# Performance work log

Hardware: AMD Instinct MI355X
Metric: run time of the kernel (lower is better)

The kernel has to match this reference:

```python
import jax, jax.numpy as jnp
import numpy as np

B, H, T = 32, 48, 24
S, A, R, F, L = 256, 64, 8, 1024, 2
EPS = 1e-5


def setup_inputs() -> dict:
    key = jax.random.key(0)
    ks = jax.random.split(key, 12)
    def w(k, shape):
        fan_in = shape[-1]
        return jax.random.normal(k, shape, jnp.float32) / jnp.sqrt(jnp.float32(fan_in))
    return {
        'history_s': jax.random.normal(ks[0], (B, H, S), jnp.float32),
        'history_a': jax.random.normal(ks[1], (B, H, A), jnp.float32),
        'present_s': jax.random.normal(ks[2], (B, S), jnp.float32),
        'future_s': jax.random.normal(ks[3], (B, T, S), jnp.float32),
        'future_a': jax.random.normal(ks[4], (B, T, A), jnp.float32),
        'W_state': w(ks[5], (F, S)), 'b_state': jnp.zeros((F,), jnp.float32),
        'g_sn': jnp.ones((F,), jnp.float32), 'b_sn': jnp.zeros((F,), jnp.float32),
        'W_action': w(ks[6], (F, A)), 'b_action': jnp.zeros((F,), jnp.float32),
        'g_an': jnp.ones((F,), jnp.float32), 'b_an': jnp.zeros((F,), jnp.float32),
        'gru_Wi': w(ks[7], (L, 3 * F, F)), 'gru_Wh': w(ks[8], (L, 3 * F, F)),
        'gru_bi': jnp.zeros((L, 3 * F), jnp.float32), 'gru_bh': jnp.zeros((L, 3 * F), jnp.float32),
        'W_reward': w(ks[9], (R, F)), 'b_reward': jnp.zeros((R,), jnp.float32),
        'W_sout': w(ks[10], (S, F)), 'b_sout': jnp.zeros((S,), jnp.float32),
    }


def _ln(x, g, b):
    m = jnp.mean(x, axis=-1, keepdims=True)
    v = jnp.mean(jnp.square(x - m), axis=-1, keepdims=True)
    return (x - m) / jnp.sqrt(v + EPS) * g + b


def _gelu(x):
    return jax.nn.gelu(x, approximate=False)  # torch F.gelu default = exact erf


def _gru_step(Wi, Wh, bi, bh, hs, x):
    # hs: [L,B,F] hidden per layer; x: [B,F]. PyTorch GRU cell semantics.
    new_hs = []
    inp = x
    for l in range(Wi.shape[0]):
        gi = inp @ Wi[l].T + bi[l]      # [B,3F]
        gh = hs[l] @ Wh[l].T + bh[l]    # [B,3F]
        ir, iz, inn = jnp.split(gi, 3, axis=-1)
        hr, hz, hn = jnp.split(gh, 3, axis=-1)
        r = jax.nn.sigmoid(ir + hr)
        z = jax.nn.sigmoid(iz + hz)
        n = jnp.tanh(inn + r * hn)
        h_new = (1.0 - z) * n + z * hs[l]
        new_hs.append(h_new)
        inp = h_new  # dropout between layers is identity (drop_rate=0)
    return jnp.stack(new_hs), inp


def reference(history_s, history_a, present_s, future_s, future_a,
              W_state, b_state, g_sn, b_sn, W_action, b_action, g_an, b_an,
              gru_Wi, gru_Wh, gru_bi, gru_bh, W_reward, b_reward, W_sout, b_sout):
    # Original forward() reruns the GRU from scratch over a growing window each
    # future step; since h0=0 this is mathematically identical to carrying the
    # hidden state incrementally (module's own _forward variant), which we do.
    Bv = history_s.shape[0]
    Fv = W_state.shape[0]
    Lv = gru_Wi.shape[0]

    hs = _ln(history_s @ W_state.T + b_state, g_sn, b_sn)   # [B,H,F]
    ha = _ln(history_a @ W_action.T + b_action, g_an, b_an)  # [B,H,F]
    ps = _ln(present_s @ W_state.T + b_state, g_sn, b_sn)    # [B,F]
    fa = _ln(future_a @ W_action.T + b_action, g_an, b_an)   # [B,T,F]

    hist_sa = hs + ha  # [B,H,F]

    def head(y):
        r = jnp.tanh(y @ W_reward.T + b_reward)
        s = y @ W_sout.T + b_sout  # state_activation is identity
        return r, s

    # step 0: full window = history + (present + future_a[0])
    seq0 = _gelu(jnp.concatenate([hist_sa, (ps + fa[:, 0])[:, None, :]], axis=1))
    h0 = jnp.zeros((Lv, Bv, Fv), seq0.dtype)

    def scan_seq(h, x):
        h, y = _gru_step(gru_Wi, gru_Wh, gru_bi, gru_bh, h, x)
        return h, y

    hT, ys = jax.lax.scan(scan_seq, h0, jnp.swapaxes(seq0, 0, 1))  # ys: [H+1,B,F]
    r0, s0 = head(ys[-1])
    pres = _ln(s0 @ W_state.T + b_state, g_sn, b_sn)

    def scan_fut(carry, fa_t):
        h, p = carry
        x = _gelu(p + fa_t)  # [B,F]
        h, y = _gru_step(gru_Wi, gru_Wh, gru_bi, gru_bh, h, x)
        r, s = head(y)
        p_new = _ln(s @ W_state.T + b_state, g_sn, b_sn)
        return (h, p_new), (r, s)

    _, (rs, ss) = jax.lax.scan(scan_fut, (hT, pres), jnp.swapaxes(fa[:, 1:], 0, 1))
    future_r = jnp.concatenate([r0[:, None], jnp.swapaxes(rs, 0, 1)], axis=1)  # [B,T,R]
    future_s_out = jnp.concatenate([s0[:, None], jnp.swapaxes(ss, 0, 1)], axis=1)  # [B,T,S]
    return future_r, future_s_out
```

## Files before the change

### kernel.cpp

```cpp
#include <hip/hip_runtime.h>
#include <cmath>

constexpr int kB = 32, kH = 48, kT = 24, kS = 256, kA = 64, kR = 8, kF = 1024;
constexpr int kSEQ = kH + 1;
constexpr float kEPS = 1e-5f;

constexpr int G  = 128;
constexpr int BT = 512;

typedef __attribute__((ext_vector_type(8))) short short8;
typedef __attribute__((ext_vector_type(4))) float f32x4;

union U4S8 { uint4 u; short8 s; };

__device__ __forceinline__ unsigned bfbits(float x) {
  unsigned u = __float_as_uint(x);
  return (u + 0x7fffu + ((u >> 16) & 1u)) >> 16;
}
__device__ __forceinline__ float bf_lo(unsigned u) { return __uint_as_float(u << 16); }
__device__ __forceinline__ float bf_hi(unsigned u) { return __uint_as_float(u & 0xffff0000u); }
__device__ __forceinline__ float bf2f(unsigned short h) {
  return __uint_as_float(((unsigned)h) << 16);
}
__device__ __forceinline__ float gelu_f(float x) {
  return 0.5f * x * (1.0f + erff(x * 0.7071067811865476f));
}
__device__ __forceinline__ float sigmoid_f(float x) {
  return 1.0f / (1.0f + expf(-x));
}

__device__ __forceinline__ void coh_st(unsigned* p, unsigned v) {
  __hip_atomic_store(p, v, __ATOMIC_RELAXED, __HIP_MEMORY_SCOPE_AGENT);
}

__device__ __forceinline__ void wwait(const unsigned* line, unsigned tgt) {
  for (;;) {
    unsigned v;
    asm volatile("global_load_dword %0, %1, off sc0 sc1\n\t"
                 "s_waitcnt vmcnt(0)"
                 : "=v"(v) : "v"(line) : "memory");
    if (v >= tgt) break;
    __builtin_amdgcn_s_sleep(1);
  }
}
__device__ __forceinline__ void wait4(const unsigned* fl,
                                      unsigned t0, unsigned t1,
                                      unsigned t2, unsigned t3) {
  if (threadIdx.x == 0) {
    for (;;) {
      unsigned a, b, c, d;
      asm volatile(
        "global_load_dword %0, %4, off sc0 sc1\n\t"
        "global_load_dword %1, %5, off sc0 sc1\n\t"
        "global_load_dword %2, %6, off sc0 sc1\n\t"
        "global_load_dword %3, %7, off sc0 sc1\n\t"
        "s_waitcnt vmcnt(0)"
        : "=&v"(a), "=&v"(b), "=&v"(c), "=&v"(d)
        : "v"(fl), "v"(fl + 32), "v"(fl + 64), "v"(fl + 96)
        : "memory");
      if (a >= t0 && b >= t1 && c >= t2 && d >= t3) break;
      __builtin_amdgcn_s_sleep(1);
    }
  }
  __syncthreads();
}
__device__ __forceinline__ void sig_oct(unsigned* fl, int fb) {
  if (threadIdx.x == 0)
    __hip_atomic_fetch_add(fl + ((fb >> 3) & 7) * 32, 1u,
                           __ATOMIC_RELAXED, __HIP_MEMORY_SCOPE_AGENT);
}
__device__ __forceinline__ void sig16(unsigned* fl, int b) {
  if (threadIdx.x == 0)
    __hip_atomic_fetch_add(fl + ((b >> 4) & 1) * 32, 1u,
                           __ATOMIC_RELAXED, __HIP_MEMORY_SCOPE_AGENT);
}

__device__ __forceinline__ void layer_stage(
    const unsigned short* __restrict__ xsrc,
    const unsigned short* __restrict__ hsrc,
    unsigned short* __restrict__ hdst,
    const unsigned* xw8,
    const unsigned* hw8,
    const unsigned* xblk2,
    int hfirst,
    const short8 (&Bf)[2][3][4],
    float bR, float bZ, float bIN, float bHN,
    float& h_old, float* part, int fb)
{
  const int tid = threadIdx.x;
  const int wv = tid >> 6, l = tid & 63, q = l >> 4, c = l & 15;

  short8 Ax[2][4], Ah[2][4];
  const int base = c*1024 + wv*128 + q*8;

  if (hfirst) {
    if (hw8) wwait(hw8 + wv*32, 8u);
    #pragma unroll
    for (int mt = 0; mt < 2; mt++)
      #pragma unroll
      for (int j = 0; j < 4; j++)
        Ah[mt][j] = *(const short8*)(hsrc + base + mt*16*1024 + j*32);
    if (xblk2) wait4(xblk2, 16u, 16u, 0u, 0u);
    if (xw8) wwait(xw8 + wv*32, 8u);
    #pragma unroll
    for (int mt = 0; mt < 2; mt++)
      #pragma unroll
      for (int j = 0; j < 4; j++)
        Ax[mt][j] = *(const short8*)(xsrc + base + mt*16*1024 + j*32);
  } else {
    #pragma unroll
    for (int mt = 0; mt < 2; mt++)
      #pragma unroll
      for (int j = 0; j < 4; j++)
        Ax[mt][j] = *(const short8*)(xsrc + base + mt*16*1024 + j*32);
    if (hw8) wwait(hw8 + wv*32, 8u);
    #pragma unroll
    for (int mt = 0; mt < 2; mt++)
      #pragma unroll
      for (int j = 0; j < 4; j++)
        Ah[mt][j] = *(const short8*)(hsrc + base + mt*16*1024 + j*32);
  }

  f32x4 C[4][2];
  #pragma unroll
  for (int s = 0; s < 4; s++)
    #pragma unroll
    for (int mt = 0; mt < 2; mt++)
      C[s][mt] = (f32x4){0.f, 0.f, 0.f, 0.f};

  #pragma unroll
  for (int mt = 0; mt < 2; mt++)
    #pragma unroll
    for (int j = 0; j < 4; j++) {
      C[0][mt] = __builtin_amdgcn_mfma_f32_16x16x32_bf16(Ax[mt][j], Bf[0][0][j], C[0][mt], 0, 0, 0);
      C[0][mt] = __builtin_amdgcn_mfma_f32_16x16x32_bf16(Ah[mt][j], Bf[1][0][j], C[0][mt], 0, 0, 0);
      C[1][mt] = __builtin_amdgcn_mfma_f32_16x16x32_bf16(Ax[mt][j], Bf[0][1][j], C[1][mt], 0, 0, 0);
      C[1][mt] = __builtin_amdgcn_mfma_f32_16x16x32_bf16(Ah[mt][j], Bf[1][1][j], C[1][mt], 0, 0, 0);
      C[2][mt] = __builtin_amdgcn_mfma_f32_16x16x32_bf16(Ax[mt][j], Bf[0][2][j], C[2][mt], 0, 0, 0);
      C[3][mt] = __builtin_amdgcn_mfma_f32_16x16x32_bf16(Ah[mt][j], Bf[1][2][j], C[3][mt], 0, 0, 0);
    }

  const int perm = (wv + l + (l >> 3)) & 7;
  #pragma unroll
  for (int s = 0; s < 4; s++)
    #pragma unroll
    for (int mt = 0; mt < 2; mt++)
      #pragma unroll
      for (int r = 0; r < 4; r++)
        part[((s*2 + mt)*4 + r)*512 + l*8 + perm] = C[s][mt][r];
  __syncthreads();

  const int mt_c = wv & 1, rg = wv >> 1;
  const int b_own = mt_c*16 + q*4 + rg;
  float S[4];
  #pragma unroll
  for (int s = 0; s < 4; s++) {
    const float* pp = part + ((s*2 + mt_c)*4 + rg)*512 + l*8;
    f32x4 a = *(const f32x4*)pp;
    f32x4 b = *(const f32x4*)(pp + 4);
    S[s] = ((a[0]+a[1]) + (a[2]+a[3])) + ((b[0]+b[1]) + (b[2]+b[3]));
  }
  float rr = sigmoid_f(S[0] + bR);
  float zz = sigmoid_f(S[1] + bZ);
  float nn = tanhf(S[2] + bIN + rr * (S[3] + bHN));
  float hn = (1.f - zz)*nn + zz*h_old;
  h_old = hn;
  float nb = __shfl_xor(hn, 1);
  if (!(c & 1)) {
    unsigned pk = bfbits(hn) | (bfbits(nb) << 16);
    coh_st((unsigned*)(hdst + b_own*1024 + fb*16 + c), pk);
  }
  __syncthreads();
}

__device__ __forceinline__ void f3_stage(
    const unsigned short* __restrict__ y_bf, int t,
    const unsigned short* __restrict__ WsT2_bf, const float* __restrict__ b_sout,
    const unsigned short* __restrict__ Wr_bf, const float* __restrict__ b_reward,
    const unsigned short* __restrict__ WstT_bf, const float* __restrict__ b_state,
    const float* __restrict__ g_sn, const float* __restrict__ b_sn,
    const unsigned short* __restrict__ fa_bf,
    float* __restrict__ out_r, float* __restrict__ out_s,
    unsigned short* __restrict__ xbuf_bf, float* part, int b)
{
  const int tid = threadIdx.x;
  float* yb    = part;
  float* spart = part + 1024;
  float* s_sh  = part + 1536;
  float* rpart = part + 1792;
  float* red1  = part + 2048;
  float* red2  = part + 2560;

  {
    unsigned uu = *((const unsigned*)y_bf + b*512 + tid);
    yb[tid*2]     = bf_lo(uu);
    yb[tid*2 + 1] = bf_hi(uu);
  }
  __syncthreads();
  {
    const int j = tid & 255, ksh = tid >> 8;
    const unsigned* wp = (const unsigned*)WsT2_bf + (size_t)ksh*256*256 + j;
    const float* yp = yb + ksh*512;
    float acc = 0.f;
    #pragma unroll 8
    for (int kp = 0; kp < 256; kp++) {
      unsigned w = wp[kp*256];
      acc += bf_lo(w)*yp[2*kp] + bf_hi(w)*yp[2*kp + 1];
    }
    spart[tid] = acc;
  }
  __syncthreads();
  if (tid < 256) {
    float s = spart[tid] + spart[tid + 256] + b_sout[tid];
    out_s[((size_t)b*kT + t)*kS + tid] = s;
    s_sh[tid] = s;
  } else if (tid < 320) {
    const int idx = tid - 256, j = idx >> 3, ks = idx & 7;
    const unsigned short* wr = Wr_bf + j*1024 + ks*128;
    const float* yp = yb + ks*128;
    float acc = 0.f;
    #pragma unroll 4
    for (int k = 0; k < 128; k += 2) {
      unsigned w = *(const unsigned*)(wr + k);
      acc += bf_lo(w)*yp[k] + bf_hi(w)*yp[k+1];
    }
    rpart[idx] = acc;
  }
  __syncthreads();
  if (tid < 8) {
    float a = b_reward[tid];
    #pragma unroll
    for (int ks = 0; ks < 8; ks++) a += rpart[tid*8 + ks];
    out_r[((size_t)b*kT + t)*kR + tid] = tanhf(a);
  }
  if (t == kT - 1) return;
  __syncthreads();
  const int f0 = tid*2;
  float a0 = b_state[f0], a1 = b_state[f0 + 1];
  {
    const unsigned* wp = (const unsigned*)WstT_bf + (f0 >> 1);
    #pragma unroll 8
    for (int k = 0; k < 256; k++) {
      unsigned w = wp[k*512];
      a0 += bf_lo(w)*s_sh[k];
      a1 += bf_hi(w)*s_sh[k];
    }
  }
  float s1 = a0 + a1, s2 = a0*a0 + a1*a1;
  red1[tid] = s1; red2[tid] = s2;
  __syncthreads();
  for (int off = 256; off > 0; off >>= 1) {
    if (tid < off) { red1[tid] += red1[tid + off]; red2[tid] += red2[tid + off]; }
    __syncthreads();
  }
  const float mean = red1[0] * (1.0f/kF);
  const float var  = red2[0] * (1.0f/kF) - mean*mean;
  const float inv  = rsqrtf(var + kEPS);
  unsigned fu = *((const unsigned*)(fa_bf + ((size_t)(t+1)*kB + b)*kF) + tid);
  float x0 = (a0 - mean)*inv*g_sn[f0]   + b_sn[f0]   + bf_lo(fu);
  float x1 = (a1 - mean)*inv*g_sn[f0+1] + b_sn[f0+1] + bf_hi(fu);
  unsigned pk = bfbits(gelu_f(x0)) | (bfbits(gelu_f(x1)) << 16);
  coh_st((unsigned*)xbuf_bf + b*512 + tid, pk);
}

__device__ __forceinline__ void load_bfrags(
    const float* __restrict__ gru_Wi, const float* __restrict__ gru_Wh,
    int lay, int fb, int wv, int q, int c, short8 (&Bf)[2][3][4])
{
  const size_t WLL = (size_t)3 * kF * kF;
  const float* Wm[2] = { gru_Wi + lay*WLL, gru_Wh + lay*WLL };
  #pragma unroll
  for (int m = 0; m < 2; m++)
    #pragma unroll
    for (int g = 0; g < 3; g++)
      #pragma unroll
      for (int j = 0; j < 4; j++) {
        const float* p = Wm[m] + ((size_t)(g*kF + fb*16 + c))*kF + wv*128 + j*32 + q*8;
        float4 a = *(const float4*)p;
        float4 b = *(const float4*)(p + 4);
        U4S8 u;
        u.u.x = bfbits(a.x) | (bfbits(a.y) << 16);
        u.u.y = bfbits(a.z) | (bfbits(a.w) << 16);
        u.u.z = bfbits(b.x) | (bfbits(b.y) << 16);
        u.u.w = bfbits(b.z) | (bfbits(b.w) << 16);
        Bf[m][g][j] = u.s;
      }
}

__global__ __launch_bounds__(BT, 2) void gru_hist(
    const float* __restrict__ gru_Wi, const float* __restrict__ gru_Wh,
    const float* __restrict__ gru_bi, const float* __restrict__ gru_bh,
    const unsigned short* __restrict__ seq0_bf,
    unsigned short* h0pool, unsigned short* h1pool,
    unsigned* hflags)
{
  __shared__ float part[32 * 512];
  const int tid = threadIdx.x;
  const int blk = blockIdx.x;
  const int wv = tid >> 6, l = tid & 63, q = l >> 4, c = l & 15;
  const bool isL1 = (blk >= 64);
  const int fb = blk & 63;
  const int lay = isL1 ? 1 : 0;
  const size_t BF = (size_t)kB * kF;

  short8 Bf[2][3][4];
  load_bfrags(gru_Wi, gru_Wh, lay, fb, wv, q, c, Bf);
  const int f = fb*16 + c;
  const float* bi = gru_bi + lay*3*kF;
  const float* bh = gru_bh + lay*3*kF;
  const float bR  = bi[f] + bh[f];
  const float bZ  = bi[kF + f] + bh[kF + f];
  const float bIN = bi[2*kF + f];
  const float bHN = bh[2*kF + f];

  float h_old = 0.f;

  #define H0P(i) (h0pool + (size_t)(i)*BF)
  #define H1P(i) (h1pool + (size_t)(i)*BF)
  #define FH0(s) (hflags + (size_t)((s) - 1) * 256)
  #define FH1(s) (hflags + (size_t)(48 + (s)) * 256)

  for (int s = 0; s < 50; s++) {
    if (!isL1) {
      if (s < 49) {
        layer_stage(seq0_bf + (size_t)s*BF, H0P(s), H0P(s+1),
                    nullptr, (s >= 1) ? FH0(s) : nullptr, nullptr, 0,
                    Bf, bR, bZ, bIN, bHN, h_old, part, fb);
        sig_oct(FH0(s+1), fb);
      }
    } else {
      if (s >= 1) {
        layer_stage(H0P(s), H1P(s-1), H1P(s),
                    FH0(s), (s >= 2) ? FH1(s-1) : nullptr, nullptr, 1,
                    Bf, bR, bZ, bIN, bHN, h_old, part, fb);
        sig_oct(FH1(s), fb);
      }
    }
  }
  #undef H0P
  #undef H1P
  #undef FH0
  #undef FH1
}

__global__ __launch_bounds__(BT, 2) void gru_fut(
    const float* __restrict__ gru_Wi, const float* __restrict__ gru_Wh,
    const float* __restrict__ gru_bi, const float* __restrict__ gru_bh,
    const unsigned short* __restrict__ WsT2_bf, const float* __restrict__ b_sout,
    const unsigned short* __restrict__ Wr_bf, const float* __restrict__ b_reward,
    const unsigned short* __restrict__ WstT_bf, const float* __restrict__ b_state,
    const float* __restrict__ g_sn, const float* __restrict__ b_sn,
    const unsigned short* __restrict__ fa_bf,
    unsigned short* h0pool, unsigned short* h1pool, unsigned short* xbpool,
    unsigned* fflags,
    float* __restrict__ out_r, float* __restrict__ out_s)
{
  __shared__ float part[32 * 512];
  const int tid = threadIdx.x;
  const int blk = blockIdx.x;
  const int wv = tid >> 6, l = tid & 63, q = l >> 4, c = l & 15;
  const bool isL1 = (blk >= 64);
  const int fb = blk & 63;
  const int lay = isL1 ? 1 : 0;
  const size_t BF = (size_t)kB * kF;

  short8 Bf[2][3][4];
  load_bfrags(gru_Wi, gru_Wh, lay, fb, wv, q, c, Bf);
  const int f = fb*16 + c;
  const float* bi = gru_bi + lay*3*kF;
  const float* bh = gru_bh + lay*3*kF;
  const float bR  = bi[f] + bh[f];
  const float bZ  = bi[kF + f] + bh[kF + f];
  const float bIN = bi[2*kF + f];
  const float bHN = bh[2*kF + f];

  #define H0P(i) (h0pool + (size_t)(i)*BF)
  #define H1P(i) (h1pool + (size_t)(i)*BF)
  #define XBP(i) (xbpool + (size_t)(i)*BF)
  #define FH0F(t) (fflags + (size_t)(t) * 256)
  #define FH1F(t) (fflags + (size_t)(23 + (t)) * 256)
  #define FXF(t)  (fflags + (size_t)46 * 256 + (size_t)(t) * 64)

  const int b_own = (wv & 1)*16 + q*4 + (wv >> 1);
  float h_old;
  {
    const unsigned short* hs = isL1 ? H1P(49) : H0P(49);
    h_old = bf2f(hs[b_own*1024 + f]);
  }

  for (int t = 0; t < kT; t++) {
    if (blk < kB) {
      if (t >= 1) {
        wait4(FH1F(t-1), 8u, 8u, 8u, 8u);
        wait4(FH1F(t-1) + 128, 8u, 8u, 8u, 8u);
      }
      f3_stage(H1P(49+t), t, WsT2_bf, b_sout, Wr_bf, b_reward,
               WstT_bf, b_state, g_sn, b_sn, fa_bf,
               out_r, out_s, XBP(t), part, blk);
      if (t < kT - 1) { __syncthreads(); sig16(FXF(t), blk); }
    }
    if (t == kT - 1) break;
    if (!isL1) {
      layer_stage(XBP(t), H0P(49+t), H0P(50+t),
                  nullptr, (t >= 1) ? FH0F(t-1) : nullptr, FXF(t), 1,
                  Bf, bR, bZ, bIN, bHN, h_old, part, fb);
      sig_oct(FH0F(t), fb);
    } else {
      layer_stage(H0P(50+t), H1P(49+t), H1P(50+t),
                  FH0F(t), (t >= 1) ? FH1F(t-1) : nullptr, nullptr, 1,
                  Bf, bR, bZ, bIN, bHN, h_old, part, fb);
      sig_oct(FH1F(t), fb);
    }
  }
  #undef H0P
  #undef H1P
  #undef XBP
  #undef FH0F
  #undef FH1F
  #undef FXF
}

__global__ __launch_bounds__(512) void convert_weights(
    const float* __restrict__ ws,  unsigned short* __restrict__ wsT2,
    const float* __restrict__ wst, unsigned short* __restrict__ wstT,
    const float* __restrict__ wr,  unsigned short* __restrict__ o3)
{
  const int stride = gridDim.x * blockDim.x;
  const int i0 = blockIdx.x * blockDim.x + threadIdx.x;
  for (int i = i0; i < kS*kF; i += stride) {
    const int j = i >> 10, k = i & 1023;
    wsT2[(k >> 1)*512 + j*2 + (k & 1)] = (unsigned short)bfbits(ws[i]);
  }
  for (int i = i0; i < kF*kS; i += stride) {
    const int ff = i >> 8, k = i & 255;
    wstT[k*1024 + ff] = (unsigned short)bfbits(wst[i]);
  }
  for (int i = i0; i < kR*kF; i += stride) o3[i] = (unsigned short)bfbits(wr[i]);
}

__global__ __launch_bounds__(256) void encode_fa_kernel(
    const float* __restrict__ future_a,
    const float* __restrict__ W_action, const float* __restrict__ b_action,
    const float* __restrict__ g_an, const float* __restrict__ b_an,
    unsigned short* __restrict__ fa_bf)
{
  __shared__ __align__(16) float arow[kA];
  __shared__ float red1[256], red2[256];
  const int bid = blockIdx.x;
  const int b = bid & (kB - 1);
  const int t = bid >> 5;
  const int tid = threadIdx.x;
  if (tid < kA) arow[tid] = future_a[((size_t)b*kT + t)*kA + tid];
  __syncthreads();
  float v[4]; float s1 = 0.f, s2 = 0.f;
  #pragma unroll
  for (int j = 0; j < 4; j++) {
    const int ff = tid + j*256;
    const float* wr = W_action + (size_t)ff*kA;
    float acc = b_action[ff];
    for (int k = 0; k < kA; k += 4) {
      float4 w  = *(const float4*)(wr + k);
      float4 xv = *(const float4*)(arow + k);
      acc += xv.x*w.x + xv.y*w.y + xv.z*w.z + xv.w*w.w;
    }
    v[j] = acc; s1 += acc; s2 += acc*acc;
  }
  red1[tid] = s1; red2[tid] = s2;
  __syncthreads();
  for (int off = 128; off > 0; off >>= 1) {
    if (tid < off) { red1[tid] += red1[tid+off]; red2[tid] += red2[tid+off]; }
    __syncthreads();
  }
  const float m = red1[0] * (1.0f/kF);
  const float va = red2[0] * (1.0f/kF) - m*m;
  const float inv = rsqrtf(va + kEPS);
  #pragma unroll
  for (int j = 0; j < 4; j++) {
    const int ff = tid + j*256;
    fa_bf[((size_t)t*kB + b)*kF + ff] =
        (unsigned short)bfbits((v[j] - m)*inv*g_an[ff] + b_an[ff]);
  }
}

__global__ __launch_bounds__(256) void encode_seq0_kernel(
    const float* __restrict__ history_s, const float* __restrict__ history_a,
    const float* __restrict__ present_s,
    const float* __restrict__ W_state, const float* __restrict__ b_state,
    const float* __restrict__ g_sn, const float* __restrict__ b_sn,
    const float* __restrict__ W_action, const float* __restrict__ b_action,
    const float* __restrict__ g_an, const float* __restrict__ b_an,
    const unsigned short* __restrict__ fa_bf, unsigned short* __restrict__ seq0_bf)
{
  __shared__ __align__(16) float srow[kS];
  __shared__ __align__(16) float arow[kA];
  __shared__ float red1[256], red2[256];
  const int bid = blockIdx.x;
  const int b = bid & (kB - 1);
  const int t = bid >> 5;
  const int tid = threadIdx.x;
  const bool hist = (t < kH);
  const float* sp = hist ? (history_s + ((size_t)b*kH + t)*kS)
                         : (present_s + (size_t)b*kS);
  srow[tid] = sp[tid];
  if (hist && tid < kA) arow[tid] = history_a[((size_t)b*kH + t)*kA + tid];
  __syncthreads();

  float u[4]; float s1 = 0.f, s2 = 0.f;
  #pragma unroll
  for (int j = 0; j < 4; j++) {
    const int ff = tid + j*256;
    const float* wr = W_state + (size_t)ff*kS;
    float acc = b_state[ff];
    for (int k = 0; k < kS; k += 4) {
      float4 w  = *(const float4*)(wr + k);
      float4 xv = *(const float4*)(srow + k);
      acc += xv.x*w.x + xv.y*w.y + xv.z*w.z + xv.w*w.w;
    }
    u[j] = acc; s1 += acc; s2 += acc*acc;
  }
  red1[tid] = s1; red2[tid] = s2;
  __syncthreads();
  for (int off = 128; off > 0; off >>= 1) {
    if (tid < off) { red1[tid] += red1[tid+off]; red2[tid] += red2[tid+off]; }
    __syncthreads();
  }
  const float mu = red1[0] * (1.0f/kF);
  const float vu = red2[0] * (1.0f/kF) - mu*mu;
  const float iu = rsqrtf(vu + kEPS);
  __syncthreads();

  if (hist) {
    float v[4]; s1 = 0.f; s2 = 0.f;
    #pragma unroll
    for (int j = 0; j < 4; j++) {
      const int ff = tid + j*256;
      const float* wr = W_action + (size_t)ff*kA;
      float acc = b_action[ff];
      for (int k = 0; k < kA; k += 4) {
        float4 w  = *(const float4*)(wr + k);
        float4 xv = *(const float4*)(arow + k);
        acc += xv.x*w.x + xv.y*w.y + xv.z*w.z + xv.w*w.w;
      }
      v[j] = acc; s1 += acc; s2 += acc*acc;
    }
    red1[tid] = s1; red2[tid] = s2;
    __syncthreads();
    for (int off = 128; off > 0; off >>= 1) {
      if (tid < off) { red1[tid] += red1[tid+off]; red2[tid] += red2[tid+off]; }
      __syncthreads();
    }
    const float mv = red1[0] * (1.0f/kF);
    const float vv = red2[0] * (1.0f/kF) - mv*mv;
    const float iv = rsqrtf(vv + kEPS);
    #pragma unroll
    for (int j = 0; j < 4; j++) {
      const int ff = tid + j*256;
      const float un = (u[j] - mu)*iu*g_sn[ff] + b_sn[ff];
      const float vn = (v[j] - mv)*iv*g_an[ff] + b_an[ff];
      seq0_bf[((size_t)t*kB + b)*kF + ff] = (unsigned short)bfbits(gelu_f(un + vn));
    }
  } else {
    #pragma unroll
    for (int j = 0; j < 4; j++) {
      const int ff = tid + j*256;
      const float un = (u[j] - mu)*iu*g_sn[ff] + b_sn[ff];
      seq0_bf[((size_t)t*kB + b)*kF + ff] =
          (unsigned short)bfbits(gelu_f(un + bf2f(fa_bf[(size_t)b*kF + ff])));
    }
  }
}

extern "C" void kernel_launch(void* const* d_in, const int* in_sizes, int n_in,
                              void* d_out, int out_size, void* d_ws, size_t ws_size,
                              hipStream_t stream) {
  (void)in_sizes; (void)n_in; (void)out_size;
  const float* history_s = (const float*)d_in[0];
  const float* history_a = (const float*)d_in[1];
  const float* present_s = (const float*)d_in[2];
  const float* future_a  = (const float*)d_in[4];
  const float* W_state   = (const float*)d_in[5];
  const float* b_state   = (const float*)d_in[6];
  const float* g_sn      = (const float*)d_in[7];
  const float* b_sn      = (const float*)d_in[8];
  const float* W_action  = (const float*)d_in[9];
  const float* b_action  = (const float*)d_in[10];
  const float* g_an      = (const float*)d_in[11];
  const float* b_an      = (const float*)d_in[12];
  const float* gru_Wi    = (const float*)d_in[13];
  const float* gru_Wh    = (const float*)d_in[14];
  const float* gru_bi    = (const float*)d_in[15];
  const float* gru_bh    = (const float*)d_in[16];
  const float* W_reward  = (const float*)d_in[17];
  const float* b_reward  = (const float*)d_in[18];
  const float* W_sout    = (const float*)d_in[19];
  const float* b_sout    = (const float*)d_in[20];

  char* ws = (char*)d_ws;
  unsigned short* seq0_bf = (unsigned short*)(ws + 0);
  unsigned short* fa_bf   = (unsigned short*)(ws + 3211264);
  unsigned short* WsT2_bf = (unsigned short*)(ws + 4784128);
  unsigned short* WstT_bf = (unsigned short*)(ws + 5308416);
  unsigned short* Wr_bf   = (unsigned short*)(ws + 5832704);
  unsigned short* h0pool  = (unsigned short*)(ws + 5849088);
  unsigned short* h1pool  = (unsigned short*)(ws + 10633216);
  unsigned short* xbpool  = (unsigned short*)(ws + 15417344);
  unsigned*       hflags  = (unsigned*)(ws + 16924672);
  unsigned*       fflags  = (unsigned*)(ws + 17025024);
  const size_t need = 17078016;
  if (ws_size < need) return;

  hipMemsetAsync((void*)h0pool, 0, 65536, stream);
  hipMemsetAsync((void*)h1pool, 0, 65536, stream);
  hipMemsetAsync((void*)hflags, 0, 100352 + 52992, stream);

  float* out_r = (float*)d_out;
  float* out_s = out_r + (size_t)kB*kT*kR;

  hipLaunchKernelGGL(convert_weights, dim3(256), dim3(512), 0, stream,
                     W_sout, WsT2_bf, W_state, WstT_bf, W_reward, Wr_bf);
  hipLaunchKernelGGL(encode_fa_kernel, dim3(kT*kB), dim3(256), 0, stream,
                     future_a, W_action, b_action, g_an, b_an, fa_bf);
  hipLaunchKernelGGL(encode_seq0_kernel, dim3(kSEQ*kB), dim3(256), 0, stream,
                     history_s, history_a, present_s,
                     W_state, b_state, g_sn, b_sn,
                     W_action, b_action, g_an, b_an, fa_bf, seq0_bf);
  hipLaunchKernelGGL(gru_hist, dim3(G), dim3(BT), 0, stream,
                     gru_Wi, gru_Wh, gru_bi, gru_bh,
                     seq0_bf, h0pool, h1pool, hflags);
  hipLaunchKernelGGL(gru_fut, dim3(G), dim3(BT), 0, stream,
                     gru_Wi, gru_Wh, gru_bi, gru_bh,
                     WsT2_bf, b_sout, Wr_bf, b_reward, WstT_bf, b_state,
                     g_sn, b_sn, fa_bf,
                     h0pool, h1pool, xbpool, fflags,
                     out_r, out_s);
}
```

Measured before the change: 1.472 ms.

## Fuse head/state feedback into layer-0 blocks with MFMA and defer outputs

The future-step feedback path (y→s→state projection→LayerNorm→GELU) no longer runs in 32 dedicated blocks that signal the layer-0 blocks through a global buffer and flags. Each layer-0 block now recomputes it redundantly for all 32 batches using bf16 MFMA in LDS, which removes one cross-block synchronisation hop per timestep. Output heads for s and r are computed after the recurrence by otherwise idle blocks, overlapped with the remaining steps. The cost is much more redundant per-block compute and weight reads on the critical path, and occupancy drops to one block per CU.

```diff
diff --git a/kernel.cpp b/kernel.cpp
--- a/kernel.cpp
+++ b/kernel.cpp
@@ -27,6 +27,15 @@
 }
 __device__ __forceinline__ float sigmoid_f(float x) {
   return 1.0f / (1.0f + expf(-x));
+}
+__device__ __forceinline__ float dot8bb(const unsigned short* w, const unsigned short* y) {
+  uint4 a = *(const uint4*)w; uint4 b = *(const uint4*)y;
+  float r = 0.f;
+  r += bf_lo(a.x)*bf_lo(b.x); r += bf_hi(a.x)*bf_hi(b.x);
+  r += bf_lo(a.y)*bf_lo(b.y); r += bf_hi(a.y)*bf_hi(b.y);
+  r += bf_lo(a.z)*bf_lo(b.z); r += bf_hi(a.z)*bf_hi(b.z);
+  r += bf_lo(a.w)*bf_lo(b.w); r += bf_hi(a.w)*bf_hi(b.w);
+  return r;
 }
 
 __device__ __forceinline__ void coh_st(unsigned* p, unsigned v) {
@@ -69,19 +78,12 @@
     __hip_atomic_fetch_add(fl + ((fb >> 3) & 7) * 32, 1u,
                            __ATOMIC_RELAXED, __HIP_MEMORY_SCOPE_AGENT);
 }
-__device__ __forceinline__ void sig16(unsigned* fl, int b) {
-  if (threadIdx.x == 0)
-    __hip_atomic_fetch_add(fl + ((b >> 4) & 1) * 32, 1u,
-                           __ATOMIC_RELAXED, __HIP_MEMORY_SCOPE_AGENT);
-}
 
 __device__ __forceinline__ void layer_stage(
     const unsigned short* __restrict__ xsrc,
     const unsigned short* __restrict__ hsrc,
     unsigned short* __restrict__ hdst,
-    const unsigned* xw8,
-    const unsigned* hw8,
-    const unsigned* xblk2,
+    const unsigned* xw8, const unsigned* hw8,
     int hfirst,
     const short8 (&Bf)[2][3][4],
     float bR, float bZ, float bIN, float bHN,
@@ -100,7 +102,6 @@
       #pragma unroll
       for (int j = 0; j < 4; j++)
         Ah[mt][j] = *(const short8*)(hsrc + base + mt*16*1024 + j*32);
-    if (xblk2) wait4(xblk2, 16u, 16u, 0u, 0u);
     if (xw8) wwait(xw8 + wv*32, 8u);
     #pragma unroll
     for (int mt = 0; mt < 2; mt++)
@@ -171,96 +172,6 @@
     coh_st((unsigned*)(hdst + b_own*1024 + fb*16 + c), pk);
   }
   __syncthreads();
-}
-
-__device__ __forceinline__ void f3_stage(
-    const unsigned short* __restrict__ y_bf, int t,
-    const unsigned short* __restrict__ WsT2_bf, const float* __restrict__ b_sout,
-    const unsigned short* __restrict__ Wr_bf, const float* __restrict__ b_reward,
-    const unsigned short* __restrict__ WstT_bf, const float* __restrict__ b_state,
-    const float* __restrict__ g_sn, const float* __restrict__ b_sn,
-    const unsigned short* __restrict__ fa_bf,
-    float* __restrict__ out_r, float* __restrict__ out_s,
-    unsigned short* __restrict__ xbuf_bf, float* part, int b)
-{
-  const int tid = threadIdx.x;
-  float* yb    = part;
-  float* spart = part + 1024;
-  float* s_sh  = part + 1536;
-  float* rpart = part + 1792;
-  float* red1  = part + 2048;
-  float* red2  = part + 2560;
-
-  {
-    unsigned uu = *((const unsigned*)y_bf + b*512 + tid);
-    yb[tid*2]     = bf_lo(uu);
-    yb[tid*2 + 1] = bf_hi(uu);
-  }
-  __syncthreads();
-  {
-    const int j = tid & 255, ksh = tid >> 8;
-    const unsigned* wp = (const unsigned*)WsT2_bf + (size_t)ksh*256*256 + j;
-    const float* yp = yb + ksh*512;
-    float acc = 0.f;
-    #pragma unroll 8
-    for (int kp = 0; kp < 256; kp++) {
-      unsigned w = wp[kp*256];
-      acc += bf_lo(w)*yp[2*kp] + bf_hi(w)*yp[2*kp + 1];
-    }
-    spart[tid] = acc;
-  }
-  __syncthreads();
-  if (tid < 256) {
-    float s = spart[tid] + spart[tid + 256] + b_sout[tid];
-    out_s[((size_t)b*kT + t)*kS + tid] = s;
-    s_sh[tid] = s;
-  } else if (tid < 320) {
-    const int idx = tid - 256, j = idx >> 3, ks = idx & 7;
-    const unsigned short* wr = Wr_bf + j*1024 + ks*128;
-    const float* yp = yb + ks*128;
-    float acc = 0.f;
-    #pragma unroll 4
-    for (int k = 0; k < 128; k += 2) {
-      unsigned w = *(const unsigned*)(wr + k);
-      acc += bf_lo(w)*yp[k] + bf_hi(w)*yp[k+1];
-    }
-    rpart[idx] = acc;
-  }
-  __syncthreads();
-  if (tid < 8) {
-    float a = b_reward[tid];
-    #pragma unroll
-    for (int ks = 0; ks < 8; ks++) a += rpart[tid*8 + ks];
-    out_r[((size_t)b*kT + t)*kR + tid] = tanhf(a);
-  }
-  if (t == kT - 1) return;
-  __syncthreads();
-  const int f0 = tid*2;
-  float a0 = b_state[f0], a1 = b_state[f0 + 1];
-  {
-    const unsigned* wp = (const unsigned*)WstT_bf + (f0 >> 1);
-    #pragma unroll 8
-    for (int k = 0; k < 256; k++) {
-      unsigned w = wp[k*512];
-      a0 += bf_lo(w)*s_sh[k];
-      a1 += bf_hi(w)*s_sh[k];
-    }
-  }
-  float s1 = a0 + a1, s2 = a0*a0 + a1*a1;
-  red1[tid] = s1; red2[tid] = s2;
-  __syncthreads();
-  for (int off = 256; off > 0; off >>= 1) {
-    if (tid < off) { red1[tid] += red1[tid + off]; red2[tid] += red2[tid + off]; }
-    __syncthreads();
-  }
-  const float mean = red1[0] * (1.0f/kF);
-  const float var  = red2[0] * (1.0f/kF) - mean*mean;
-  const float inv  = rsqrtf(var + kEPS);
-  unsigned fu = *((const unsigned*)(fa_bf + ((size_t)(t+1)*kB + b)*kF) + tid);
-  float x0 = (a0 - mean)*inv*g_sn[f0]   + b_sn[f0]   + bf_lo(fu);
-  float x1 = (a1 - mean)*inv*g_sn[f0+1] + b_sn[f0+1] + bf_hi(fu);
-  unsigned pk = bfbits(gelu_f(x0)) | (bfbits(gelu_f(x1)) << 16);
-  coh_st((unsigned*)xbuf_bf + b*512 + tid, pk);
 }
 
 __device__ __forceinline__ void load_bfrags(
@@ -324,14 +235,14 @@
     if (!isL1) {
       if (s < 49) {
         layer_stage(seq0_bf + (size_t)s*BF, H0P(s), H0P(s+1),
-                    nullptr, (s >= 1) ? FH0(s) : nullptr, nullptr, 0,
+                    nullptr, (s >= 1) ? FH0(s) : nullptr, 0,
                     Bf, bR, bZ, bIN, bHN, h_old, part, fb);
         sig_oct(FH0(s+1), fb);
       }
     } else {
       if (s >= 1) {
         layer_stage(H0P(s), H1P(s-1), H1P(s),
-                    FH0(s), (s >= 2) ? FH1(s-1) : nullptr, nullptr, 1,
+                    FH0(s), (s >= 2) ? FH1(s-1) : nullptr, 1,
                     Bf, bR, bZ, bIN, bHN, h_old, part, fb);
         sig_oct(FH1(s), fb);
       }
@@ -343,19 +254,20 @@
   #undef FH1
 }
 
-__global__ __launch_bounds__(BT, 2) void gru_fut(
+__global__ __launch_bounds__(BT, 1) void gru_fut(
     const float* __restrict__ gru_Wi, const float* __restrict__ gru_Wh,
     const float* __restrict__ gru_bi, const float* __restrict__ gru_bh,
-    const unsigned short* __restrict__ WsT2_bf, const float* __restrict__ b_sout,
+    const unsigned short* __restrict__ Ws_bf, const float* __restrict__ b_sout,
     const unsigned short* __restrict__ Wr_bf, const float* __restrict__ b_reward,
-    const unsigned short* __restrict__ WstT_bf, const float* __restrict__ b_state,
+    const unsigned short* __restrict__ Wst_bf, const float* __restrict__ b_state,
     const float* __restrict__ g_sn, const float* __restrict__ b_sn,
     const unsigned short* __restrict__ fa_bf,
-    unsigned short* h0pool, unsigned short* h1pool, unsigned short* xbpool,
+    unsigned short* h0pool, unsigned short* h1pool,
     unsigned* fflags,
     float* __restrict__ out_r, float* __restrict__ out_s)
 {
   __shared__ float part[32 * 512];
+  unsigned short* lds_bf = (unsigned short*)part;
   const int tid = threadIdx.x;
   const int blk = blockIdx.x;
   const int wv = tid >> 6, l = tid & 63, q = l >> 4, c = l & 15;
@@ -376,10 +288,8 @@
 
   #define H0P(i) (h0pool + (size_t)(i)*BF)
   #define H1P(i) (h1pool + (size_t)(i)*BF)
-  #define XBP(i) (xbpool + (size_t)(i)*BF)
   #define FH0F(t) (fflags + (size_t)(t) * 256)
   #define FH1F(t) (fflags + (size_t)(23 + (t)) * 256)
-  #define FXF(t)  (fflags + (size_t)46 * 256 + (size_t)(t) * 64)
 
   const int b_own = (wv & 1)*16 + q*4 + (wv >> 1);
   float h_old;
@@ -388,53 +298,307 @@
     h_old = bf2f(hs[b_own*1024 + f]);
   }
 
-  for (int t = 0; t < kT; t++) {
-    if (blk < kB) {
-      if (t >= 1) {
-        wait4(FH1F(t-1), 8u, 8u, 8u, 8u);
-        wait4(FH1F(t-1) + 128, 8u, 8u, 8u, 8u);
-      }
-      f3_stage(H1P(49+t), t, WsT2_bf, b_sout, Wr_bf, b_reward,
-               WstT_bf, b_state, g_sn, b_sn, fa_bf,
-               out_r, out_s, XBP(t), part, blk);
-      if (t < kT - 1) { __syncthreads(); sig16(FXF(t), blk); }
-    }
-    if (t == kT - 1) break;
+  for (int t = 0; t < kT - 1; t++) {
     if (!isL1) {
-      layer_stage(XBP(t), H0P(49+t), H0P(50+t),
-                  nullptr, (t >= 1) ? FH0F(t-1) : nullptr, FXF(t), 1,
-                  Bf, bR, bZ, bIN, bHN, h_old, part, fb);
+      const unsigned short* ysrc = H1P(49+t);
+      if (t >= 1) wwait(FH1F(t-1) + wv*32, 8u);
+      #pragma unroll
+      for (int i = 0; i < 8; i++) {
+        const int cidx = l + 64*i;
+        const int b = cidx >> 4, kc = cidx & 15;
+        const int k = wv*128 + kc*8;
+        uint4 v = *(const uint4*)(ysrc + b*1024 + k);
+        *(uint4*)(lds_bf + b*1024 + (k ^ ((b & 7) << 3))) = v;
+      }
+      short8 Ah[2][4];
+      {
+        if (t >= 1) wwait(FH0F(t-1) + wv*32, 8u);
+        const unsigned short* hsrc = H0P(49+t);
+        #pragma unroll
+        for (int mt = 0; mt < 2; mt++)
+          #pragma unroll
+          for (int j = 0; j < 4; j++)
+            Ah[mt][j] = *(const short8*)(hsrc + (mt*16 + c)*1024 + wv*128 + j*32 + q*8);
+      }
+      __syncthreads();
+
+      f32x4 Cs[2][2];
+      Cs[0][0] = Cs[0][1] = Cs[1][0] = Cs[1][1] = (f32x4){0.f,0.f,0.f,0.f};
+      for (int ks = 0; ks < 32; ks++) {
+        short8 By[2];
+        #pragma unroll
+        for (int bt = 0; bt < 2; bt++) {
+          const int b = bt*16 + c;
+          const int k = ks*32 + q*8;
+          By[bt] = *(const short8*)(lds_bf + b*1024 + (k ^ ((b & 7) << 3)));
+        }
+        #pragma unroll
+        for (int jt = 0; jt < 2; jt++) {
+          short8 Aw = *(const short8*)(Ws_bf + (size_t)(wv*32 + jt*16 + c)*1024 + ks*32 + q*8);
+          Cs[jt][0] = __builtin_amdgcn_mfma_f32_16x16x32_bf16(Aw, By[0], Cs[jt][0], 0, 0, 0);
+          Cs[jt][1] = __builtin_amdgcn_mfma_f32_16x16x32_bf16(Aw, By[1], Cs[jt][1], 0, 0, 0);
+        }
+      }
+      __syncthreads();
+
+      #pragma unroll
+      for (int jt = 0; jt < 2; jt++) {
+        const int jbase = wv*32 + jt*16 + q*4;
+        const float4 bs = *(const float4*)(b_sout + jbase);
+        #pragma unroll
+        for (int bt = 0; bt < 2; bt++) {
+          const int b = bt*16 + c;
+          uint2 pk;
+          pk.x = bfbits(Cs[jt][bt][0] + bs.x) | (bfbits(Cs[jt][bt][1] + bs.y) << 16);
+          pk.y = bfbits(Cs[jt][bt][2] + bs.z) | (bfbits(Cs[jt][bt][3] + bs.w) << 16);
+          *(uint2*)(lds_bf + b*256 + (jbase ^ ((b & 7) << 3))) = pk;
+        }
+      }
+      __syncthreads();
+
+      f32x4 Cu[8][2];
+      #pragma unroll
+      for (int ft = 0; ft < 8; ft++) {
+        Cu[ft][0] = (f32x4){0.f,0.f,0.f,0.f};
+        Cu[ft][1] = (f32x4){0.f,0.f,0.f,0.f};
+      }
+      for (int ks = 0; ks < 8; ks++) {
+        short8 Bs2[2];
+        #pragma unroll
+        for (int nt = 0; nt < 2; nt++) {
+          const int b = nt*16 + c;
+          const int k = ks*32 + q*8;
+          Bs2[nt] = *(const short8*)(lds_bf + b*256 + (k ^ ((b & 7) << 3)));
+        }
+        #pragma unroll
+        for (int ft = 0; ft < 8; ft++) {
+          short8 Aw = *(const short8*)(Wst_bf + (size_t)(wv*128 + ft*16 + c)*256 + ks*32 + q*8);
+          Cu[ft][0] = __builtin_amdgcn_mfma_f32_16x16x32_bf16(Aw, Bs2[0], Cu[ft][0], 0, 0, 0);
+          Cu[ft][1] = __builtin_amdgcn_mfma_f32_16x16x32_bf16(Aw, Bs2[1], Cu[ft][1], 0, 0, 0);
+        }
+      }
+      float s1a[2] = {0.f, 0.f}, s2a[2] = {0.f, 0.f};
+      #pragma unroll
+      for (int ft = 0; ft < 8; ft++) {
+        const int f0 = wv*128 + ft*16 + q*4;
+        const float4 bst = *(const float4*)(b_state + f0);
+        #pragma unroll
+        for (int nt = 0; nt < 2; nt++) {
+          Cu[ft][nt][0] += bst.x; Cu[ft][nt][1] += bst.y;
+          Cu[ft][nt][2] += bst.z; Cu[ft][nt][3] += bst.w;
+          #pragma unroll
+          for (int r = 0; r < 4; r++) {
+            const float u = Cu[ft][nt][r];
+            s1a[nt] += u; s2a[nt] += u*u;
+          }
+        }
+      }
+      #pragma unroll
+      for (int nt = 0; nt < 2; nt++) {
+        s1a[nt] += __shfl_xor(s1a[nt], 16); s2a[nt] += __shfl_xor(s2a[nt], 16);
+        s1a[nt] += __shfl_xor(s1a[nt], 32); s2a[nt] += __shfl_xor(s2a[nt], 32);
+      }
+      if (q == 0) {
+        #pragma unroll
+        for (int nt = 0; nt < 2; nt++) {
+          part[4096 + (wv*32 + nt*16 + c)*2]     = s1a[nt];
+          part[4096 + (wv*32 + nt*16 + c)*2 + 1] = s2a[nt];
+        }
+      }
+      __syncthreads();
+      if (tid < 32) {
+        float S1 = 0.f, S2 = 0.f;
+        #pragma unroll
+        for (int w = 0; w < 8; w++) {
+          S1 += part[4096 + (w*32 + tid)*2];
+          S2 += part[4096 + (w*32 + tid)*2 + 1];
+        }
+        const float mean = S1 * (1.0f/kF);
+        const float var  = S2 * (1.0f/kF) - mean*mean;
+        part[4608 + tid*2]     = mean;
+        part[4608 + tid*2 + 1] = rsqrtf(var + kEPS);
+      }
+      __syncthreads();
+      float mn[2], iv[2];
+      #pragma unroll
+      for (int nt = 0; nt < 2; nt++) {
+        mn[nt] = part[4608 + (nt*16 + c)*2];
+        iv[nt] = part[4608 + (nt*16 + c)*2 + 1];
+      }
+      __syncthreads();
+
+      #pragma unroll
+      for (int ft = 0; ft < 8; ft++) {
+        const int f0 = wv*128 + ft*16 + q*4;
+        const float4 g4 = *(const float4*)(g_sn + f0);
+        const float4 b4 = *(const float4*)(b_sn + f0);
+        #pragma unroll
+        for (int nt = 0; nt < 2; nt++) {
+          const int b = nt*16 + c;
+          const unsigned* fap = (const unsigned*)(fa_bf + ((size_t)(t+1)*kB + b)*kF + f0);
+          const unsigned fu0 = fap[0], fu1 = fap[1];
+          float x0 = gelu_f((Cu[ft][nt][0] - mn[nt])*iv[nt]*g4.x + b4.x + bf_lo(fu0));
+          float x1 = gelu_f((Cu[ft][nt][1] - mn[nt])*iv[nt]*g4.y + b4.y + bf_hi(fu0));
+          float x2 = gelu_f((Cu[ft][nt][2] - mn[nt])*iv[nt]*g4.z + b4.z + bf_lo(fu1));
+          float x3 = gelu_f((Cu[ft][nt][3] - mn[nt])*iv[nt]*g4.w + b4.w + bf_hi(fu1));
+          uint2 pk;
+          pk.x = bfbits(x0) | (bfbits(x1) << 16);
+          pk.y = bfbits(x2) | (bfbits(x3) << 16);
+          *(uint2*)(lds_bf + b*1024 + (f0 ^ ((b & 7) << 3))) = pk;
+        }
+      }
+      __syncthreads();
+
+      short8 Ax[2][4];
+      #pragma unroll
+      for (int mt = 0; mt < 2; mt++)
+        #pragma unroll
+        for (int j = 0; j < 4; j++) {
+          const int b = mt*16 + c;
+          const int k = wv*128 + j*32 + q*8;
+          Ax[mt][j] = *(const short8*)(lds_bf + b*1024 + (k ^ ((b & 7) << 3)));
+        }
+      f32x4 C[4][2];
+      #pragma unroll
+      for (int s = 0; s < 4; s++)
+        #pragma unroll
+        for (int mt = 0; mt < 2; mt++)
+          C[s][mt] = (f32x4){0.f, 0.f, 0.f, 0.f};
+      #pragma unroll
+      for (int mt = 0; mt < 2; mt++)
+        #pragma unroll
+        for (int j = 0; j < 4; j++) {
+          C[0][mt] = __builtin_amdgcn_mfma_f32_16x16x32_bf16(Ax[mt][j], Bf[0][0][j], C[0][mt], 0, 0, 0);
+          C[0][mt] = __builtin_amdgcn_mfma_f32_16x16x32_bf16(Ah[mt][j], Bf[1][0][j], C[0][mt], 0, 0, 0);
+          C[1][mt] = __builtin_amdgcn_mfma_f32_16x16x32_bf16(Ax[mt][j], Bf[0][1][j], C[1][mt], 0, 0, 0);
+          C[1][mt] = __builtin_amdgcn_mfma_f32_16x16x32_bf16(Ah[mt][j], Bf[1][1][j], C[1][mt], 0, 0, 0);
+          C[2][mt] = __builtin_amdgcn_mfma_f32_16x16x32_bf16(Ax[mt][j], Bf[0][2][j], C[2][mt], 0, 0, 0);
+          C[3][mt] = __builtin_amdgcn_mfma_f32_16x16x32_bf16(Ah[mt][j], Bf[1][2][j], C[3][mt], 0, 0, 0);
+        }
+      __syncthreads();
+      const int perm = (wv + l + (l >> 3)) & 7;
+      #pragma unroll
+      for (int s = 0; s < 4; s++)
+        #pragma unroll
+        for (int mt = 0; mt < 2; mt++)
+          #pragma unroll
+          for (int r = 0; r < 4; r++)
+            part[((s*2 + mt)*4 + r)*512 + l*8 + perm] = C[s][mt][r];
+      __syncthreads();
+      const int mt_c = wv & 1, rg = wv >> 1;
+      float S[4];
+      #pragma unroll
+      for (int s = 0; s < 4; s++) {
+        const float* pp = part + ((s*2 + mt_c)*4 + rg)*512 + l*8;
+        f32x4 a = *(const f32x4*)pp;
+        f32x4 b = *(const f32x4*)(pp + 4);
+        S[s] = ((a[0]+a[1]) + (a[2]+a[3])) + ((b[0]+b[1]) + (b[2]+b[3]));
+      }
+      float rr2 = sigmoid_f(S[0] + bR);
+      float zz = sigmoid_f(S[1] + bZ);
+      float nn = tanhf(S[2] + bIN + rr2 * (S[3] + bHN));
+      float hn = (1.f - zz)*nn + zz*h_old;
+      h_old = hn;
+      float nb = __shfl_xor(hn, 1);
+      if (!(c & 1)) {
+        unsigned pk = bfbits(hn) | (bfbits(nb) << 16);
+        coh_st((unsigned*)(H0P(50+t) + b_own*1024 + fb*16 + c), pk);
+      }
+      __syncthreads();
       sig_oct(FH0F(t), fb);
     } else {
       layer_stage(H0P(50+t), H1P(49+t), H1P(50+t),
-                  FH0F(t), (t >= 1) ? FH1F(t-1) : nullptr, nullptr, 1,
+                  FH0F(t), (t >= 1) ? FH1F(t-1) : nullptr, 1,
                   Bf, bR, bZ, bIN, bHN, h_old, part, fb);
       sig_oct(FH1F(t), fb);
     }
   }
+
+  if (blk < 96) {
+    const int t = blk >> 2, jq = blk & 3;
+    if (t >= 1) {
+      wait4(FH1F(t-1), 8u, 8u, 8u, 8u);
+      wait4(FH1F(t-1) + 128, 8u, 8u, 8u, 8u);
+    } else {
+      __syncthreads();
+    }
+    const unsigned short* y = H1P(49 + t);
+    short8 Ay[2][4], Bs[4][4];
+    #pragma unroll
+    for (int j = 0; j < 4; j++) {
+      const int koff = wv*128 + j*32 + q*8;
+      Ay[0][j] = *(const short8*)(y + c*1024 + koff);
+      Ay[1][j] = *(const short8*)(y + (16 + c)*1024 + koff);
+      #pragma unroll
+      for (int g = 0; g < 4; g++)
+        Bs[g][j] = *(const short8*)(Ws_bf + (size_t)(jq*64 + g*16 + c)*1024 + koff);
+    }
+    f32x4 C[4][2];
+    #pragma unroll
+    for (int g = 0; g < 4; g++) {
+      C[g][0] = (f32x4){0.f,0.f,0.f,0.f};
+      C[g][1] = (f32x4){0.f,0.f,0.f,0.f};
+    }
+    #pragma unroll
+    for (int j = 0; j < 4; j++)
+      #pragma unroll
+      for (int g = 0; g < 4; g++) {
+        C[g][0] = __builtin_amdgcn_mfma_f32_16x16x32_bf16(Ay[0][j], Bs[g][j], C[g][0], 0, 0, 0);
+        C[g][1] = __builtin_amdgcn_mfma_f32_16x16x32_bf16(Ay[1][j], Bs[g][j], C[g][1], 0, 0, 0);
+      }
+    const int perm = (wv + l + (l >> 3)) & 7;
+    #pragma unroll
+    for (int g = 0; g < 4; g++)
+      #pragma unroll
+      for (int mt = 0; mt < 2; mt++)
+        #pragma unroll
+        for (int r = 0; r < 4; r++)
+          part[((g*2 + mt)*4 + r)*512 + l*8 + perm] = C[g][mt][r];
+    __syncthreads();
+    const int mt_c = wv & 1, rg = wv >> 1;
+    const int bo = mt_c*16 + q*4 + rg;
+    #pragma unroll
+    for (int g = 0; g < 4; g++) {
+      const float* pp = part + ((g*2 + mt_c)*4 + rg)*512 + l*8;
+      f32x4 a = *(const f32x4*)pp;
+      f32x4 b2 = *(const f32x4*)(pp + 4);
+      float S = ((a[0]+a[1]) + (a[2]+a[3])) + ((b2[0]+b2[1]) + (b2[2]+b2[3]));
+      const int col = jq*64 + g*16 + c;
+      out_s[((size_t)bo*kT + t)*kS + col] = S + b_sout[col];
+    }
+  } else if (blk < 96 + kT) {
+    const int t = blk - 96;
+    if (t >= 1) {
+      wait4(FH1F(t-1), 8u, 8u, 8u, 8u);
+      wait4(FH1F(t-1) + 128, 8u, 8u, 8u, 8u);
+    }
+    const unsigned short* y = H1P(49 + t);
+    const int idx = tid >> 1, half = tid & 1;
+    const int b = idx >> 3, j = idx & 7;
+    const unsigned short* wr = Wr_bf + j*1024 + half*512;
+    const unsigned short* yp = y + b*1024 + half*512;
+    float acc = 0.f;
+    #pragma unroll 8
+    for (int k = 0; k < 512; k += 8) acc += dot8bb(wr + k, yp + k);
+    acc += __shfl_xor(acc, 1);
+    if (half == 0)
+      out_r[((size_t)b*kT + t)*kR + j] = tanhf(acc + b_reward[j]);
+  }
   #undef H0P
   #undef H1P
-  #undef XBP
   #undef FH0F
   #undef FH1F
-  #undef FXF
 }
 
 __global__ __launch_bounds__(512) void convert_weights(
-    const float* __restrict__ ws,  unsigned short* __restrict__ wsT2,
-    const float* __restrict__ wst, unsigned short* __restrict__ wstT,
+    const float* __restrict__ ws,  unsigned short* __restrict__ o1,
+    const float* __restrict__ wst, unsigned short* __restrict__ o2,
     const float* __restrict__ wr,  unsigned short* __restrict__ o3)
 {
   const int stride = gridDim.x * blockDim.x;
   const int i0 = blockIdx.x * blockDim.x + threadIdx.x;
-  for (int i = i0; i < kS*kF; i += stride) {
-    const int j = i >> 10, k = i & 1023;
-    wsT2[(k >> 1)*512 + j*2 + (k & 1)] = (unsigned short)bfbits(ws[i]);
-  }
-  for (int i = i0; i < kF*kS; i += stride) {
-    const int ff = i >> 8, k = i & 255;
-    wstT[k*1024 + ff] = (unsigned short)bfbits(wst[i]);
-  }
+  for (int i = i0; i < kS*kF; i += stride) o1[i] = (unsigned short)bfbits(ws[i]);
+  for (int i = i0; i < kF*kS; i += stride) o2[i] = (unsigned short)bfbits(wst[i]);
   for (int i = i0; i < kR*kF; i += stride) o3[i] = (unsigned short)bfbits(wr[i]);
 }
 
@@ -598,26 +762,25 @@
   char* ws = (char*)d_ws;
   unsigned short* seq0_bf = (unsigned short*)(ws + 0);
   unsigned short* fa_bf   = (unsigned short*)(ws + 3211264);
-  unsigned short* WsT2_bf = (unsigned short*)(ws + 4784128);
-  unsigned short* WstT_bf = (unsigned short*)(ws + 5308416);
+  unsigned short* Ws_bf   = (unsigned short*)(ws + 4784128);
+  unsigned short* Wst_bf  = (unsigned short*)(ws + 5308416);
   unsigned short* Wr_bf   = (unsigned short*)(ws + 5832704);
   unsigned short* h0pool  = (unsigned short*)(ws + 5849088);
   unsigned short* h1pool  = (unsigned short*)(ws + 10633216);
-  unsigned short* xbpool  = (unsigned short*)(ws + 15417344);
-  unsigned*       hflags  = (unsigned*)(ws + 16924672);
-  unsigned*       fflags  = (unsigned*)(ws + 17025024);
-  const size_t need = 17078016;
+  unsigned*       hflags  = (unsigned*)(ws + 15417344);
+  unsigned*       fflags  = (unsigned*)(ws + 15517696);
+  const size_t need = 15564800;
   if (ws_size < need) return;
 
   hipMemsetAsync((void*)h0pool, 0, 65536, stream);
   hipMemsetAsync((void*)h1pool, 0, 65536, stream);
-  hipMemsetAsync((void*)hflags, 0, 100352 + 52992, stream);
+  hipMemsetAsync((void*)hflags, 0, 100352 + 47104, stream);
 
   float* out_r = (float*)d_out;
   float* out_s = out_r + (size_t)kB*kT*kR;
 
   hipLaunchKernelGGL(convert_weights, dim3(256), dim3(512), 0, stream,
-                     W_sout, WsT2_bf, W_state, WstT_bf, W_reward, Wr_bf);
+                     W_sout, Ws_bf, W_state, Wst_bf, W_reward, Wr_bf);
   hipLaunchKernelGGL(encode_fa_kernel, dim3(kT*kB), dim3(256), 0, stream,
                      future_a, W_action, b_action, g_an, b_an, fa_bf);
   hipLaunchKernelGGL(encode_seq0_kernel, dim3(kSEQ*kB), dim3(256), 0, stream,
@@ -629,8 +792,8 @@
                      seq0_bf, h0pool, h1pool, hflags);
   hipLaunchKernelGGL(gru_fut, dim3(G), dim3(BT), 0, stream,
                      gru_Wi, gru_Wh, gru_bi, gru_bh,
-                     WsT2_bf, b_sout, Wr_bf, b_reward, WstT_bf, b_state,
+                     Ws_bf, b_sout, Wr_bf, b_reward, Wst_bf, b_state,
                      g_sn, b_sn, fa_bf,
-                     h0pool, h1pool, xbpool, fflags,
+                     h0pool, h1pool, fflags,
                      out_r, out_s);
 }
```

Result: slower. 2.737 ms (+86.0%).
